# Kernel tuning notes

Measured on AMD Instinct MI355X. Metric: run time of the kernel, lower is better.

## Reference

```python
import jax, jax.numpy as jnp
import numpy as np

D = 256        # node/edge feature dim
H = 256        # MLP hidden dim
NG = 80000     # grid (src) nodes
NM = 20000     # mesh (dst) nodes
E = 160000     # g2m edges
EPS = 1e-5


def _mlp(x, W1, b1, W2, b2, g, beta):
    # MeshGraphMLP with hidden_layers=1: Linear -> SiLU -> Linear -> LayerNorm
    h = jax.nn.silu(x @ W1 + b1)
    y = h @ W2 + b2
    mu = jnp.mean(y, axis=-1, keepdims=True)
    var = jnp.var(y, axis=-1, keepdims=True)
    return (y - mu) * jax.lax.rsqrt(var + EPS) * g + beta


def setup_inputs() -> dict:
    key = jax.random.key(0)
    ks = jax.random.split(key, 16)

    def rn(k, shape, s=0.02):
        return jax.random.normal(k, shape, dtype=jnp.float32) * s

    inp = {
        "g2m_efeat": jax.random.normal(ks[0], (E, D), dtype=jnp.float32),
        "grid_nfeat": jax.random.normal(ks[1], (NG, D), dtype=jnp.float32),
        "mesh_nfeat": jax.random.normal(ks[2], (NM, D), dtype=jnp.float32),
        "src_idx": jax.random.randint(ks[3], (E,), 0, NG, dtype=jnp.int32),
        "dst_idx": jax.random.randint(ks[4], (E,), 0, NM, dtype=jnp.int32),
        # edge MLP (concat variant): input = [efeat | src_feat | dst_feat] -> 3D
        "eW1": rn(ks[5], (3 * D, H)), "eb1": jnp.zeros((H,), jnp.float32),
        "eW2": rn(ks[6], (H, D)),     "eb2": jnp.zeros((D,), jnp.float32),
        "eg": jnp.ones((D,), jnp.float32), "ebeta": jnp.zeros((D,), jnp.float32),
        # src node MLP: D -> H -> D
        "sW1": rn(ks[7], (D, H)), "sb1": jnp.zeros((H,), jnp.float32),
        "sW2": rn(ks[8], (H, D)), "sb2": jnp.zeros((D,), jnp.float32),
        "sg": jnp.ones((D,), jnp.float32), "sbeta": jnp.zeros((D,), jnp.float32),
        # dst node MLP: (D_agg + D_node) = 2D -> H -> D
        "dW1": rn(ks[9], (2 * D, H)), "db1": jnp.zeros((H,), jnp.float32),
        "dW2": rn(ks[10], (H, D)),    "db2": jnp.zeros((D,), jnp.float32),
        "dg": jnp.ones((D,), jnp.float32), "dbeta": jnp.zeros((D,), jnp.float32),
    }
    return inp


def reference(g2m_efeat, grid_nfeat, mesh_nfeat, src_idx, dst_idx,
              eW1, eb1, eW2, eb2, eg, ebeta,
              sW1, sb1, sW2, sb2, sg, sbeta,
              dW1, db1, dW2, db2, dg, dbeta):
    # edge MLP: gather src/dst node features, concat with edge features
    e_in = jnp.concatenate(
        [g2m_efeat, grid_nfeat[src_idx], mesh_nfeat[dst_idx]], axis=-1)  # [E, 3D]
    efeat = _mlp(e_in, eW1, eb1, eW2, eb2, eg, ebeta)                    # [E, D]
    # aggregate_and_concat: copy_e_sum scatter to dst mesh nodes, concat node feats
    agg = jax.ops.segment_sum(efeat, dst_idx, num_segments=NM)           # [NM, D]
    cat_feat = jnp.concatenate([agg, mesh_nfeat], axis=-1)               # [NM, 2D]
    mesh_out = mesh_nfeat + _mlp(cat_feat, dW1, db1, dW2, db2, dg, dbeta)
    grid_out = grid_nfeat + _mlp(grid_nfeat, sW1, sb1, sW2, sb2, sg, sbeta)
    return (grid_out, mesh_out)
```

## Files before the change

kernel.cpp:

```cpp
#include <hip/hip_runtime.h>
#include <hip/hip_bf16.h>

#define DD 256
#define NGN 80000
#define NMN 20000
#define NEE 160000

typedef unsigned short u16;
typedef __attribute__((ext_vector_type(8))) short s16x8;
typedef __attribute__((ext_vector_type(4))) short s16x4;
typedef __attribute__((ext_vector_type(4))) float f32x4;

__device__ __forceinline__ u16 f2bf(float f) {
  __hip_bfloat16 h = __float2bfloat16(f);
  union { __hip_bfloat16 h; u16 u; } v; v.h = h;
  return v.u;
}
__device__ __forceinline__ float bf2f(u16 x) {
  union { unsigned u; float f; } v; v.u = ((unsigned)x) << 16;
  return v.f;
}
__device__ __forceinline__ float silu(float x) {
  return x * __builtin_amdgcn_rcpf(1.f + __expf(-x));
}

__device__ __forceinline__ s16x8 ldsA(const u16* uni, int rowL, int cL) {
  int swz = (rowL & 7) << 4;
  s16x4 lo = *(const s16x4*)((const char*)uni + rowL * 512 + ((cL * 2) ^ swz));
  s16x4 hi = *(const s16x4*)((const char*)uni + rowL * 512 + (((cL + 16) * 2) ^ swz));
  s16x8 a;
#pragma unroll
  for (int j = 0; j < 4; ++j) { a[j] = lo[j]; a[4 + j] = hi[j]; }
  return a;
}

__global__ void pack_hist(const float* __restrict__ eW1, const float* __restrict__ eW2,
                          const float* __restrict__ sW1, const float* __restrict__ sW2,
                          const float* __restrict__ dW1, const float* __restrict__ dW2,
                          u16* __restrict__ wp, const int* __restrict__ didx,
                          int* __restrict__ cnt) {
  int bid = blockIdx.x;
  if (bid < 2304) {
    const float* W; u16* dst; int lb;
    if (bid < 768)       { W = eW1; dst = wp;              lb = bid; }
    else if (bid < 1024) { W = eW2; dst = wp + 768 * 256;  lb = bid - 768; }
    else if (bid < 1280) { W = sW1; dst = wp + 1024 * 256; lb = bid - 1024; }
    else if (bid < 1536) { W = sW2; dst = wp + 1280 * 256; lb = bid - 1280; }
    else if (bid < 2048) { W = dW1; dst = wp + 1536 * 256; lb = bid - 1536; }
    else                 { W = dW2; dst = wp + 2048 * 256; lb = bid - 2048; }
    int idx = lb * 256 + threadIdx.x;
    int i = idx & 7, lane = (idx >> 3) & 63, nt = (idx >> 9) & 15, kt = idx >> 13;
    int k = kt * 32 + 4 * (lane >> 4) + (i < 4 ? i : 12 + i);
    int n = nt * 16 + (lane & 15);
    dst[idx] = f2bf(W[(size_t)k * 256 + n]);
  } else {
    int i = (bid - 2304) * 256 + threadIdx.x;
    if (i < NEE) atomicAdd(cnt + didx[i], 1);
  }
}

__global__ void csr_scan(const int* __restrict__ cnt, int* __restrict__ cursor) {
  __shared__ int psum[256];
  const int CH = (NMN + 255) / 256;
  int t = threadIdx.x;
  int base = t * CH, s = 0;
  for (int k = 0; k < CH; ++k) { int i = base + k; if (i < NMN) s += cnt[i]; }
  psum[t] = s;
  __syncthreads();
  for (int off = 1; off < 256; off <<= 1) {
    int v = (t >= off) ? psum[t - off] : 0;
    __syncthreads();
    psum[t] += v;
    __syncthreads();
  }
  int run = psum[t] - s;
  for (int k = 0; k < CH; ++k) {
    int i = base + k;
    if (i < NMN) { cursor[i] = run; run += cnt[i]; }
  }
}

__device__ __forceinline__ void gemm_body(u16* uni, const float* __restrict__ X,
                                          const u16* __restrict__ Wp, u16* __restrict__ Y,
                                          int n, int blk) {
  const int tid = threadIdx.x;
  const int lane = tid & 63;
  const int wave = tid >> 6;
  const int mr = wave >> 1, nc = wave & 1;
  const int g = lane >> 4, lr = lane & 15;
  const int row0 = blk * 64;

#pragma unroll
  for (int j = 0; j < 8; ++j) {
    int e = wave * 16 + j * 2 + (lane >> 5);
    int r = min(row0 + e, n - 1);
    const float* src = X + (size_t)r * DD + (lane & 31) * 8;
    f32x4 f0 = *(const f32x4*)src;
    f32x4 f1 = *(const f32x4*)(src + 4);
    s16x8 o;
#pragma unroll
    for (int k = 0; k < 4; ++k) { o[k] = (short)f2bf(f0[k]); o[4 + k] = (short)f2bf(f1[k]); }
    int co = (lane & 31) * 8;
    *(s16x8*)((char*)uni + e * 512 + ((co * 2) ^ ((e & 7) << 4))) = o;
  }
  __syncthreads();

  const f32x4 fz = {0.f, 0.f, 0.f, 0.f};
  f32x4 acc[2][8];
#pragma unroll
  for (int mt = 0; mt < 2; ++mt)
#pragma unroll
    for (int nt = 0; nt < 8; ++nt) acc[mt][nt] = fz;

  for (int kl = 0; kl < 8; ++kl) {
    s16x8 afr[2];
#pragma unroll
    for (int mt = 0; mt < 2; ++mt) afr[mt] = ldsA(uni, mr * 32 + mt * 16 + lr, kl * 32 + 4 * g);
#pragma unroll
    for (int h = 0; h < 2; ++h) {
      s16x8 bfr[4];
#pragma unroll
      for (int q = 0; q < 4; ++q)
        bfr[q] = *(const s16x8*)(Wp + (size_t)kl * 8192 + ((nc * 8 + h * 4 + q) * 64 + lane) * 8);
#pragma unroll
      for (int q = 0; q < 4; ++q) {
        acc[0][h * 4 + q] = __builtin_amdgcn_mfma_f32_16x16x32_bf16(afr[0], bfr[q], acc[0][h * 4 + q], 0, 0, 0);
        acc[1][h * 4 + q] = __builtin_amdgcn_mfma_f32_16x16x32_bf16(afr[1], bfr[q], acc[1][h * 4 + q], 0, 0, 0);
      }
    }
  }
  __syncthreads();
#pragma unroll
  for (int mt = 0; mt < 2; ++mt)
#pragma unroll
    for (int nt = 0; nt < 8; ++nt)
#pragma unroll
      for (int i = 0; i < 4; ++i) {
        int rowL = mr * 32 + mt * 16 + 4 * g + i;
        int col = nc * 128 + nt * 16 + lr;
        *(u16*)((char*)uni + rowL * 512 + ((col * 2) ^ ((rowL & 7) << 4))) = f2bf(acc[mt][nt][i]);
      }
  __syncthreads();
#pragma unroll
  for (int rr = 0; rr < 16; ++rr) {
    int rowL = wave * 16 + rr;
    int rg = row0 + rowL;
    if (rg < n) {
      s16x4 v = *(const s16x4*)((char*)uni + rowL * 512 + ((lane * 8) ^ ((rowL & 7) << 4)));
      *(s16x4*)(Y + (size_t)rg * DD + lane * 4) = v;
    }
  }
}

template <int MODE, int K1>
__device__ __forceinline__ void mlp_body(
    u16* uni, float2 (*pstats)[2],
    const float* __restrict__ xa, const float* __restrict__ xb,
    const u16* __restrict__ W1p, const float* __restrict__ b1,
    const u16* __restrict__ W2p, const float* __restrict__ b2,
    const float* __restrict__ gam, const float* __restrict__ bet,
    const float* __restrict__ resid, float* __restrict__ out, int nrows, int blk) {
  const int tid = threadIdx.x;
  const int lane = tid & 63;
  const int wave = tid >> 6;
  const int mr = wave >> 1, nc = wave & 1;
  const int g = lane >> 4, lr = lane & 15;
  const int row0 = blk * 64;

  const f32x4 fz = {0.f, 0.f, 0.f, 0.f};
  f32x4 acc[2][8];
#pragma unroll
  for (int mt = 0; mt < 2; ++mt)
#pragma unroll
    for (int nt = 0; nt < 8; ++nt) acc[mt][nt] = fz;

#pragma unroll
  for (int region = 0; region < K1 / 256; ++region) {
    __syncthreads();
    const float* Xr = (region == 0) ? xa : xb;
#pragma unroll
    for (int j = 0; j < 8; ++j) {
      int e = wave * 16 + j * 2 + (lane >> 5);
      int r = min(row0 + e, nrows - 1);
      const float* src = Xr + (size_t)r * DD + (lane & 31) * 8;
      f32x4 f0 = *(const f32x4*)src;
      f32x4 f1 = *(const f32x4*)(src + 4);
      s16x8 o;
#pragma unroll
      for (int k = 0; k < 4; ++k) { o[k] = (short)f2bf(f0[k]); o[4 + k] = (short)f2bf(f1[k]); }
      int co = (lane & 31) * 8;
      *(s16x8*)((char*)uni + e * 512 + ((co * 2) ^ ((e & 7) << 4))) = o;
    }
    __syncthreads();
    for (int kl = 0; kl < 8; ++kl) {
      const int kt = region * 8 + kl;
      s16x8 afr[2];
#pragma unroll
      for (int mt = 0; mt < 2; ++mt) afr[mt] = ldsA(uni, mr * 32 + mt * 16 + lr, kl * 32 + 4 * g);
#pragma unroll
      for (int h = 0; h < 2; ++h) {
        s16x8 bfr[4];
#pragma unroll
        for (int q = 0; q < 4; ++q)
          bfr[q] = *(const s16x8*)(W1p + (size_t)kt * 8192 + ((nc * 8 + h * 4 + q) * 64 + lane) * 8);
#pragma unroll
        for (int q = 0; q < 4; ++q) {
          acc[0][h * 4 + q] = __builtin_amdgcn_mfma_f32_16x16x32_bf16(afr[0], bfr[q], acc[0][h * 4 + q], 0, 0, 0);
          acc[1][h * 4 + q] = __builtin_amdgcn_mfma_f32_16x16x32_bf16(afr[1], bfr[q], acc[1][h * 4 + q], 0, 0, 0);
        }
      }
    }
  }
  __syncthreads();

  {
    float b1v[8];
#pragma unroll
    for (int nt = 0; nt < 8; ++nt) b1v[nt] = b1[nc * 128 + nt * 16 + lr];
#pragma unroll
    for (int mt = 0; mt < 2; ++mt)
#pragma unroll
      for (int nt = 0; nt < 8; ++nt)
#pragma unroll
        for (int i = 0; i < 4; ++i) {
          float x = acc[mt][nt][i] + b1v[nt];
          float h = silu(x);
          int rowL = mr * 32 + mt * 16 + 4 * g + i;
          int col = nc * 128 + nt * 16 + lr;
          *(u16*)((char*)uni + rowL * 512 + ((col * 2) ^ ((rowL & 7) << 4))) = f2bf(h);
        }
  }
  __syncthreads();

#pragma unroll
  for (int mt = 0; mt < 2; ++mt)
#pragma unroll
    for (int nt = 0; nt < 8; ++nt) acc[mt][nt] = fz;
  for (int kl = 0; kl < 8; ++kl) {
    s16x8 afr[2];
#pragma unroll
    for (int mt = 0; mt < 2; ++mt) afr[mt] = ldsA(uni, mr * 32 + mt * 16 + lr, kl * 32 + 4 * g);
#pragma unroll
    for (int h = 0; h < 2; ++h) {
      s16x8 bfr[4];
#pragma unroll
      for (int q = 0; q < 4; ++q)
        bfr[q] = *(const s16x8*)(W2p + (size_t)kl * 8192 + ((nc * 8 + h * 4 + q) * 64 + lane) * 8);
#pragma unroll
      for (int q = 0; q < 4; ++q) {
        acc[0][h * 4 + q] = __builtin_amdgcn_mfma_f32_16x16x32_bf16(afr[0], bfr[q], acc[0][h * 4 + q], 0, 0, 0);
        acc[1][h * 4 + q] = __builtin_amdgcn_mfma_f32_16x16x32_bf16(afr[1], bfr[q], acc[1][h * 4 + q], 0, 0, 0);
      }
    }
  }

  float b2v[8], gv[8], bv[8];
#pragma unroll
  for (int nt = 0; nt < 8; ++nt) {
    int col = nc * 128 + nt * 16 + lr;
    b2v[nt] = b2[col];
    gv[nt] = gam[col];
    bv[nt] = bet[col];
  }
#pragma unroll
  for (int mt = 0; mt < 2; ++mt)
#pragma unroll
    for (int i = 0; i < 4; ++i) {
      float s = 0.f, s2 = 0.f;
#pragma unroll
      for (int nt = 0; nt < 8; ++nt) {
        float y = acc[mt][nt][i] + b2v[nt];
        s += y;
        s2 += y * y;
      }
#pragma unroll
      for (int m = 1; m < 16; m <<= 1) {
        s += __shfl_xor(s, m);
        s2 += __shfl_xor(s2, m);
      }
      if (lr == 0) pstats[mr * 32 + mt * 16 + 4 * g + i][nc] = make_float2(s, s2);
    }
  __syncthreads();
#pragma unroll
  for (int mt = 0; mt < 2; ++mt)
#pragma unroll
    for (int i = 0; i < 4; ++i) {
      int rowL = mr * 32 + mt * 16 + 4 * g + i;
      float2 pa = pstats[rowL][0], pb = pstats[rowL][1];
      float sum = pa.x + pb.x, sq = pa.y + pb.y;
      float mu = sum * (1.f / 256.f);
      float var = fmaxf(sq * (1.f / 256.f) - mu * mu, 0.f);
      float rs = rsqrtf(var + 1e-5f);
      int rg = row0 + rowL;
      if (MODE == 2 && rg >= nrows) continue;
#pragma unroll
      for (int nt = 0; nt < 8; ++nt) {
        int col = nc * 128 + nt * 16 + lr;
        float y = acc[mt][nt][i] + b2v[nt];
        float val = (y - mu) * rs * gv[nt] + bv[nt];
        out[(size_t)rg * DD + col] = resid[(size_t)rg * DD + col] + val;
      }
    }
}

__global__ __launch_bounds__(256, 3) void gemm_fill(
    const float* __restrict__ efeat, const float* __restrict__ gridf,
    const float* __restrict__ mesh, const u16* __restrict__ wp,
    u16* __restrict__ ECp, u16* __restrict__ GSp, u16* __restrict__ GMp,
    const int* __restrict__ didx, int* __restrict__ cursor, int* __restrict__ eids,
    const float* __restrict__ sb1, const float* __restrict__ sb2,
    const float* __restrict__ sg, const float* __restrict__ sbt,
    float* __restrict__ gout, int withMlp) {
  __shared__ u16 uni[16384];
  __shared__ float2 pstats[64][2];
  int bid = blockIdx.x;
  if (withMlp) {
    if (bid < 3750) {
      if ((bid % 3) == 2) {
        mlp_body<1, 256>(uni, pstats, gridf, nullptr, wp + 1024 * 256, sb1,
                         wp + 1280 * 256, sb2, sg, sbt, gridf, gout, NGN, bid / 3);
        return;
      }
      gemm_body(uni, efeat, wp, ECp, NEE, (bid / 3) * 2 + (bid % 3));
      return;
    }
    bid -= 1250;
  }
  if (bid < 2500) gemm_body(uni, efeat, wp, ECp, NEE, bid);
  else if (bid < 3750) gemm_body(uni, gridf, wp + 8 * 8192, GSp, NGN, bid - 2500);
  else if (bid < 4063) gemm_body(uni, mesh, wp + 16 * 8192, GMp, NMN, bid - 3750);
  else {
    int e = (bid - 4063) * 256 + threadIdx.x;
    if (e < NEE) { int p = atomicAdd(cursor + didx[e], 1); eids[p] = e; }
  }
}

__global__ __launch_bounds__(256, 3) void edge_kern(
    const u16* __restrict__ ECp, const u16* __restrict__ GSp, const u16* __restrict__ GMp,
    const int* __restrict__ sidx, const int* __restrict__ eids,
    const float* __restrict__ b1,
    const u16* __restrict__ W2p, const float* __restrict__ b2,
    const float* __restrict__ gam, const float* __restrict__ bet,
    const int* __restrict__ didx, float* __restrict__ agg) {
  __shared__ u16 uni[16384];
  __shared__ float2 pstats[64][2];
  __shared__ int eidL[64], srcL[64], dstL[64];

  const int tid = threadIdx.x;
  const int lane = tid & 63;
  const int wave = tid >> 6;
  const int mr = wave >> 1, nc = wave & 1;
  const int g = lane >> 4, lr = lane & 15;
  const int row0 = blockIdx.x * 64;

  if (tid < 64) {
    int e = eids[row0 + tid];
    eidL[tid] = e;
    srcL[tid] = sidx[e];
    dstL[tid] = didx[e];
  }
  __syncthreads();

  const int co = (lane & 31) * 8;
  f32x4 b1a = *(const f32x4*)(b1 + co);
  f32x4 b1b = *(const f32x4*)(b1 + co + 4);
#pragma unroll
  for (int j = 0; j < 8; ++j) {
    int e = wave * 16 + j * 2 + (lane >> 5);
    s16x8 va = *(const s16x8*)(ECp + (size_t)eidL[e] * DD + co);
    s16x8 vb = *(const s16x8*)(GSp + (size_t)srcL[e] * DD + co);
    s16x8 vc = *(const s16x8*)(GMp + (size_t)dstL[e] * DD + co);
    s16x8 o;
#pragma unroll
    for (int k = 0; k < 8; ++k) {
      float bk = (k < 4) ? b1a[k] : b1b[k - 4];
      float x = bf2f((u16)va[k]) + bf2f((u16)vb[k]) + bf2f((u16)vc[k]) + bk;
      o[k] = (short)f2bf(silu(x));
    }
    *(s16x8*)((char*)uni + e * 512 + ((co * 2) ^ ((e & 7) << 4))) = o;
  }
  __syncthreads();

  const f32x4 fz = {0.f, 0.f, 0.f, 0.f};
  f32x4 acc[2][8];
#pragma unroll
  for (int mt = 0; mt < 2; ++mt)
#pragma unroll
    for (int nt = 0; nt < 8; ++nt) acc[mt][nt] = fz;
  for (int kl = 0; kl < 8; ++kl) {
    s16x8 afr[2];
#pragma unroll
    for (int mt = 0; mt < 2; ++mt) afr[mt] = ldsA(uni, mr * 32 + mt * 16 + lr, kl * 32 + 4 * g);
#pragma unroll
    for (int h = 0; h < 2; ++h) {
      s16x8 bfr[4];
#pragma unroll
      for (int q = 0; q < 4; ++q)
        bfr[q] = *(const s16x8*)(W2p + (size_t)kl * 8192 + ((nc * 8 + h * 4 + q) * 64 + lane) * 8);
#pragma unroll
      for (int q = 0; q < 4; ++q) {
        acc[0][h * 4 + q] = __builtin_amdgcn_mfma_f32_16x16x32_bf16(afr[0], bfr[q], acc[0][h * 4 + q], 0, 0, 0);
        acc[1][h * 4 + q] = __builtin_amdgcn_mfma_f32_16x16x32_bf16(afr[1], bfr[q], acc[1][h * 4 + q], 0, 0, 0);
      }
    }
  }

  float b2v[8], gv[8], bv[8];
#pragma unroll
  for (int nt = 0; nt < 8; ++nt) {
    int col = nc * 128 + nt * 16 + lr;
    b2v[nt] = b2[col];
    gv[nt] = gam[col];
    bv[nt] = bet[col];
  }
#pragma unroll
  for (int mt = 0; mt < 2; ++mt)
#pragma unroll
    for (int i = 0; i < 4; ++i) {
      float s = 0.f, s2 = 0.f;
#pragma unroll
      for (int nt = 0; nt < 8; ++nt) {
        float y = acc[mt][nt][i] + b2v[nt];
        s += y;
        s2 += y * y;
      }
#pragma unroll
      for (int m = 1; m < 16; m <<= 1) {
        s += __shfl_xor(s, m);
        s2 += __shfl_xor(s2, m);
      }
      if (lr == 0) pstats[mr * 32 + mt * 16 + 4 * g + i][nc] = make_float2(s, s2);
    }
  __syncthreads();

#pragma unroll
  for (int mt = 0; mt < 2; ++mt)
#pragma unroll
    for (int i = 0; i < 4; ++i) {
      int rowL = mr * 32 + mt * 16 + 4 * g + i;
      float2 pa = pstats[rowL][0], pb = pstats[rowL][1];
      float sum = pa.x + pb.x, sq = pa.y + pb.y;
      float mu = sum * (1.f / 256.f);
      float var = fmaxf(sq * (1.f / 256.f) - mu * mu, 0.f);
      float rs = rsqrtf(var + 1e-5f);
#pragma unroll
      for (int nt = 0; nt < 8; ++nt) {
        int col = nc * 128 + nt * 16 + lr;
        float y = acc[mt][nt][i] + b2v[nt];
        float val = (y - mu) * rs * gv[nt] + bv[nt];
        *(u16*)((char*)uni + rowL * 512 + ((col * 2) ^ ((rowL & 7) << 4))) = f2bf(val);
      }
    }
  __syncthreads();

  {
    int c = tid;
    float sum = 0.f;
    int prev = dstL[0];
#pragma unroll 8
    for (int r = 0; r < 64; ++r) {
      int d = dstL[r];
      if (d != prev) {
        atomicAdd(agg + (size_t)prev * DD + c, sum);
        sum = 0.f;
        prev = d;
      }
      sum += bf2f(*(const u16*)((char*)uni + r * 512 + ((c * 2) ^ ((r & 7) << 4))));
    }
    atomicAdd(agg + (size_t)prev * DD + c, sum);
  }
}

__global__ __launch_bounds__(256, 3) void mlp12_kernel(
    const float* __restrict__ agg, const float* __restrict__ mesh,
    const u16* __restrict__ dW1p, const float* __restrict__ db1,
    const u16* __restrict__ dW2p, const float* __restrict__ db2,
    const float* __restrict__ dg, const float* __restrict__ dbt,
    float* __restrict__ mout,
    const float* __restrict__ gridf,
    const u16* __restrict__ sW1p, const float* __restrict__ sb1,
    const u16* __restrict__ sW2p, const float* __restrict__ sb2,
    const float* __restrict__ sg, const float* __restrict__ sbt,
    float* __restrict__ gout, int withMlp1) {
  __shared__ u16 uni[16384];
  __shared__ float2 pstats[64][2];
  int bid = blockIdx.x;
  if (bid < 313) {
    mlp_body<2, 512>(uni, pstats, agg, mesh, dW1p, db1, dW2p, db2, dg, dbt,
                     mesh, mout, NMN, bid);
  } else if (withMlp1) {
    mlp_body<1, 256>(uni, pstats, gridf, nullptr, sW1p, sb1, sW2p, sb2,
                     sg, sbt, gridf, gout, NGN, bid - 313);
  }
}

extern "C" void kernel_launch(void* const* d_in, const int* in_sizes, int n_in,
                              void* d_out, int out_size, void* d_ws, size_t ws_size,
                              hipStream_t stream) {
  const float* g2m  = (const float*)d_in[0];
  const float* grid = (const float*)d_in[1];
  const float* mesh = (const float*)d_in[2];
  const int* sidx = (const int*)d_in[3];
  const int* didx = (const int*)d_in[4];
  const float* eW1 = (const float*)d_in[5];
  const float* eb1 = (const float*)d_in[6];
  const float* eW2 = (const float*)d_in[7];
  const float* eb2 = (const float*)d_in[8];
  const float* eg  = (const float*)d_in[9];
  const float* ebt = (const float*)d_in[10];
  const float* sW1 = (const float*)d_in[11];
  const float* sb1 = (const float*)d_in[12];
  const float* sW2 = (const float*)d_in[13];
  const float* sb2 = (const float*)d_in[14];
  const float* sg  = (const float*)d_in[15];
  const float* sbt = (const float*)d_in[16];
  const float* dW1 = (const float*)d_in[17];
  const float* db1 = (const float*)d_in[18];
  const float* dW2 = (const float*)d_in[19];
  const float* db2 = (const float*)d_in[20];
  const float* dg  = (const float*)d_in[21];
  const float* dbt = (const float*)d_in[22];

  char* w = (char*)d_ws;
  float* agg = (float*)w;
  u16* wp = (u16*)(w + 20480000);
  int* cnt = (int*)(w + 20480000 + 1179648);
  int* cursor = cnt + 20480;
  int* eids = cursor + 20480;
  const size_t GS_OFF = 22463488;
  const size_t EC_OFF = GS_OFF + (size_t)NGN * DD * 2 + (size_t)NMN * DD * 2;
  const size_t NEED_BIG = EC_OFF + (size_t)NEE * DD * 2;

  u16* eW1p = wp;
  u16* eW2p = eW1p + 768 * 256;
  u16* sW1p = eW2p + 256 * 256;
  u16* sW2p = sW1p + 256 * 256;
  u16* dW1p = sW2p + 256 * 256;
  u16* dW2p = dW1p + 512 * 256;

  float* gout = (float*)d_out;
  float* mout = gout + (size_t)NGN * DD;

  u16* GSp = (u16*)(w + GS_OFF);
  u16* GMp = GSp + (size_t)NGN * DD;
  const bool big = ws_size >= NEED_BIG;
  u16* ECp = big ? (u16*)(w + EC_OFF) : (u16*)d_out;

  (void)hipMemsetAsync(agg, 0, 20480000, stream);
  (void)hipMemsetAsync(cnt, 0, 81920, stream);

  pack_hist<<<2304 + 625, 256, 0, stream>>>(eW1, eW2, sW1, sW2, dW1, dW2, wp, didx, cnt);
  csr_scan<<<1, 256, 0, stream>>>(cnt, cursor);

  if (big) {
    gemm_fill<<<5938, 256, 0, stream>>>(g2m, grid, mesh, wp, ECp, GSp, GMp,
                                        didx, cursor, eids,
                                        sb1, sb2, sg, sbt, gout, 1);
    edge_kern<<<2500, 256, 0, stream>>>(
        ECp, GSp, GMp, sidx, eids, eb1, eW2p, eb2, eg, ebt, didx, agg);
    mlp12_kernel<<<313, 256, 0, stream>>>(
        agg, mesh, dW1p, db1, dW2p, db2, dg, dbt, mout,
        grid, sW1p, sb1, sW2p, sb2, sg, sbt, gout, 0);
  } else {
    gemm_fill<<<4688, 256, 0, stream>>>(g2m, grid, mesh, wp, ECp, GSp, GMp,
                                        didx, cursor, eids,
                                        sb1, sb2, sg, sbt, gout, 0);
    edge_kern<<<2500, 256, 0, stream>>>(
        ECp, GSp, GMp, sidx, eids, eb1, eW2p, eb2, eg, ebt, didx, agg);
    mlp12_kernel<<<313 + 1250, 256, 0, stream>>>(
        agg, mesh, dW1p, db1, dW2p, db2, dg, dbt, mout,
        grid, sW1p, sb1, sW2p, sb2, sg, sbt, gout, 1);
  }
}
```

Baseline: 362.2 us.

## Stage fp32 GEMM inputs directly into LDS via global_load_lds, convert at fragment load

The input tile load in gemm_body now uses direct global-to-LDS 16-byte loads of fp32 rows into a 64KB swizzled LDS buffer, instead of loading through registers and converting to bf16 before the LDS store. The bf16 conversion moves into the MFMA A-fragment read. This is meant to cut VGPR pressure and the register round-trip on the load path. In exchange it doubles LDS per block, lowers launch bounds occupancy from 3 to 2 blocks, and repeats the conversion work across waves.

```diff
diff --git a/kernel.cpp b/kernel.cpp
--- a/kernel.cpp
+++ b/kernel.cpp
@@ -22,6 +22,12 @@
 }
 __device__ __forceinline__ float silu(float x) {
   return x * __builtin_amdgcn_rcpf(1.f + __expf(-x));
+}
+
+__device__ __forceinline__ void gload16(const void* g, void* l) {
+  __builtin_amdgcn_global_load_lds(
+      (const __attribute__((address_space(1))) void*)g,
+      (__attribute__((address_space(3))) void*)l, 16, 0, 0);
 }
 
 __device__ __forceinline__ s16x8 ldsA(const u16* uni, int rowL, int cL) {
@@ -80,7 +86,7 @@
   }
 }
 
-__device__ __forceinline__ void gemm_body(u16* uni, const float* __restrict__ X,
+__device__ __forceinline__ void gemm_body(char* lds, const float* __restrict__ X,
                                           const u16* __restrict__ Wp, u16* __restrict__ Y,
                                           int n, int blk) {
   const int tid = threadIdx.x;
@@ -91,17 +97,11 @@
   const int row0 = blk * 64;
 
 #pragma unroll
-  for (int j = 0; j < 8; ++j) {
-    int e = wave * 16 + j * 2 + (lane >> 5);
+  for (int t = 0; t < 16; ++t) {
+    int e = wave * 16 + t;
     int r = min(row0 + e, n - 1);
-    const float* src = X + (size_t)r * DD + (lane & 31) * 8;
-    f32x4 f0 = *(const f32x4*)src;
-    f32x4 f1 = *(const f32x4*)(src + 4);
-    s16x8 o;
-#pragma unroll
-    for (int k = 0; k < 4; ++k) { o[k] = (short)f2bf(f0[k]); o[4 + k] = (short)f2bf(f1[k]); }
-    int co = (lane & 31) * 8;
-    *(s16x8*)((char*)uni + e * 512 + ((co * 2) ^ ((e & 7) << 4))) = o;
+    const float* gsrc = X + (size_t)r * DD + ((((lane * 16) ^ ((e & 7) << 4))) >> 2);
+    gload16(gsrc, lds + e * 1024);
   }
   __syncthreads();
 
@@ -115,7 +115,17 @@
   for (int kl = 0; kl < 8; ++kl) {
     s16x8 afr[2];
 #pragma unroll
-    for (int mt = 0; mt < 2; ++mt) afr[mt] = ldsA(uni, mr * 32 + mt * 16 + lr, kl * 32 + 4 * g);
+    for (int mt = 0; mt < 2; ++mt) {
+      int row = mr * 32 + mt * 16 + lr;
+      int sw = (row & 7) << 4;
+      const char* bse = lds + row * 1024;
+      f32x4 lo = *(const f32x4*)(bse + ((kl * 128 + g * 16) ^ sw));
+      f32x4 hi = *(const f32x4*)(bse + ((kl * 128 + g * 16 + 64) ^ sw));
+      s16x8 a;
+#pragma unroll
+      for (int j = 0; j < 4; ++j) { a[j] = (short)f2bf(lo[j]); a[4 + j] = (short)f2bf(hi[j]); }
+      afr[mt] = a;
+    }
 #pragma unroll
     for (int h = 0; h < 2; ++h) {
       s16x8 bfr[4];
@@ -130,6 +140,7 @@
     }
   }
   __syncthreads();
+  u16* uni = (u16*)lds;
 #pragma unroll
   for (int mt = 0; mt < 2; ++mt)
 #pragma unroll
@@ -303,7 +314,7 @@
     }
 }
 
-__global__ __launch_bounds__(256, 3) void gemm_fill(
+__global__ __launch_bounds__(256, 2) void gemm_fill(
     const float* __restrict__ efeat, const float* __restrict__ gridf,
     const float* __restrict__ mesh, const u16* __restrict__ wp,
     u16* __restrict__ ECp, u16* __restrict__ GSp, u16* __restrict__ GMp,
@@ -311,24 +322,24 @@
     const float* __restrict__ sb1, const float* __restrict__ sb2,
     const float* __restrict__ sg, const float* __restrict__ sbt,
     float* __restrict__ gout, int withMlp) {
-  __shared__ u16 uni[16384];
+  __shared__ char ldsblob[65536];
   __shared__ float2 pstats[64][2];
   int bid = blockIdx.x;
   if (withMlp) {
     if (bid < 3750) {
       if ((bid % 3) == 2) {
-        mlp_body<1, 256>(uni, pstats, gridf, nullptr, wp + 1024 * 256, sb1,
+        mlp_body<1, 256>((u16*)ldsblob, pstats, gridf, nullptr, wp + 1024 * 256, sb1,
                          wp + 1280 * 256, sb2, sg, sbt, gridf, gout, NGN, bid / 3);
         return;
       }
-      gemm_body(uni, efeat, wp, ECp, NEE, (bid / 3) * 2 + (bid % 3));
+      gemm_body(ldsblob, efeat, wp, ECp, NEE, (bid / 3) * 2 + (bid % 3));
       return;
     }
     bid -= 1250;
   }
-  if (bid < 2500) gemm_body(uni, efeat, wp, ECp, NEE, bid);
-  else if (bid < 3750) gemm_body(uni, gridf, wp + 8 * 8192, GSp, NGN, bid - 2500);
-  else if (bid < 4063) gemm_body(uni, mesh, wp + 16 * 8192, GMp, NMN, bid - 3750);
+  if (bid < 2500) gemm_body(ldsblob, efeat, wp, ECp, NEE, bid);
+  else if (bid < 3750) gemm_body(ldsblob, gridf, wp + 8 * 8192, GSp, NGN, bid - 2500);
+  else if (bid < 4063) gemm_body(ldsblob, mesh, wp + 16 * 8192, GMp, NMN, bid - 3750);
   else {
     int e = (bid - 4063) * 256 + threadIdx.x;
     if (e < NEE) { int p = atomicAdd(cursor + didx[e], 1); eids[p] = e; }
```

Result: slower. 393.0 us (+8.5%).
